# Performance work log

Measured on AMD Instinct MI355X. Metric: run time of the kernel, lower is better.

The kernel has to match this reference:

```python
import jax, jax.numpy as jnp
import numpy as np

N_NODES = 20000
EPS_BN = 1e-5
NEG_SLOPE = 0.2


def gat_conv(x, W, att_src, att_dst, bias, src, dst, heads, out_ch, concat):
    n = x.shape[0]
    h = (x @ W).reshape(n, heads, out_ch)                       # [N,H,C]
    a_src = jnp.sum(h * att_src, axis=-1)                       # [N,H]
    a_dst = jnp.sum(h * att_dst, axis=-1)                       # [N,H]
    e = jax.nn.leaky_relu(a_src[src] + a_dst[dst], NEG_SLOPE)   # [E,H]
    # segment softmax over incoming edges of each destination node
    m = jax.ops.segment_max(e, dst, num_segments=n)             # [N,H]
    e = jnp.exp(e - m[dst])
    denom = jax.ops.segment_sum(e, dst, num_segments=n)         # [N,H]
    alpha = e / (denom[dst] + 1e-16)                            # [E,H]
    msg = alpha[:, :, None] * h[src]                            # [E,H,C]
    out = jax.ops.segment_sum(msg, dst, num_segments=n)         # [N,H,C]
    if concat:
        out = out.reshape(n, heads * out_ch)
    else:
        out = out.mean(axis=1)
    return out + bias


def batch_norm(x, gamma, beta):
    mu = x.mean(axis=0)
    var = x.var(axis=0)  # biased, matches torch normalization
    return (x - mu) * jax.lax.rsqrt(var + EPS_BN) * gamma + beta


def setup_inputs() -> dict:
    key = jax.random.key(0)
    ks = jax.random.split(key, 16)
    n, d_in, hid, heads = N_NODES, 768, 128, 8
    n_edges = 160000
    x = jax.random.normal(ks[0], (n, d_in), dtype=jnp.float32)
    edge_index = jax.random.randint(ks[1], (2, n_edges), 0, n, dtype=jnp.int64)
    s = lambda fi, fo: (2.0 / (fi + fo)) ** 0.5
    return {
        "x": x,
        "edge_index": edge_index,
        "W1": jax.random.normal(ks[2], (d_in, heads * hid), jnp.float32) * s(d_in, heads * hid),
        "att_src1": jax.random.normal(ks[3], (heads, hid), jnp.float32) * 0.1,
        "att_dst1": jax.random.normal(ks[4], (heads, hid), jnp.float32) * 0.1,
        "bias1": jnp.zeros((heads * hid,), jnp.float32),
        "bn1_g": jnp.ones((heads * hid,), jnp.float32),
        "bn1_b": jnp.zeros((heads * hid,), jnp.float32),
        "W2": jax.random.normal(ks[5], (heads * hid, hid), jnp.float32) * s(heads * hid, hid),
        "att_src2": jax.random.normal(ks[6], (1, hid), jnp.float32) * 0.1,
        "att_dst2": jax.random.normal(ks[7], (1, hid), jnp.float32) * 0.1,
        "bias2": jnp.zeros((hid,), jnp.float32),
        "bn2_g": jnp.ones((hid,), jnp.float32),
        "bn2_b": jnp.zeros((hid,), jnp.float32),
        "Wc1": jax.random.normal(ks[8], (hid, 64), jnp.float32) * s(hid, 64),
        "bc1": jnp.zeros((64,), jnp.float32),
        "Wc2": jax.random.normal(ks[9], (64, 2), jnp.float32) * s(64, 2),
        "bc2": jnp.zeros((2,), jnp.float32),
    }


def reference(x, edge_index, W1, att_src1, att_dst1, bias1, bn1_g, bn1_b,
              W2, att_src2, att_dst2, bias2, bn2_g, bn2_b,
              Wc1, bc1, Wc2, bc2):
    n = x.shape[0]
    # PyG GATConv default: add self-loops
    loops = jnp.arange(n, dtype=edge_index.dtype)
    src = jnp.concatenate([edge_index[0], loops])
    dst = jnp.concatenate([edge_index[1], loops])

    h = gat_conv(x, W1, att_src1, att_dst1, bias1, src, dst, heads=8, out_ch=128, concat=True)
    h = jax.nn.elu(batch_norm(h, bn1_g, bn1_b))
    # dropout disabled (deterministic reference)
    h = gat_conv(h, W2, att_src2, att_dst2, bias2, src, dst, heads=1, out_ch=128, concat=False)
    h = jax.nn.elu(batch_norm(h, bn2_g, bn2_b))
    h = jax.nn.elu(h @ Wc1 + bc1)
    return h @ Wc2 + bc2  # [N, 2] logits
```

## Files before the change

kernel.cpp:

```cpp
#include <hip/hip_runtime.h>
#include <stdint.h>

typedef unsigned short u16;
typedef __bf16 bf16x8 __attribute__((ext_vector_type(8)));
typedef float f32x4 __attribute__((ext_vector_type(4)));

__device__ __forceinline__ float b2f(u16 u) {
    unsigned x = ((unsigned)u) << 16;
    return __builtin_bit_cast(float, x);
}
__device__ __forceinline__ u16 f2b(float f) {
    unsigned x = __builtin_bit_cast(unsigned, f);
    x = x + 0x7fffu + ((x >> 16) & 1u);
    return (u16)(x >> 16);
}
__device__ __forceinline__ float leaky(float v) { return v > 0.f ? v : 0.2f * v; }
__device__ __forceinline__ float elu(float v) { return v > 0.f ? v : expm1f(v); }

__device__ __forceinline__ void gload16(const u16* g, u16* l) {
    __builtin_amdgcn_global_load_lds((const __attribute__((address_space(1))) void*)(const void*)g,
                                     (__attribute__((address_space(3))) void*)(void*)l, 16, 0, 0);
}

__global__ void k_cast4(const float* __restrict__ in, u16* __restrict__ out, size_t n4) {
    size_t i = blockIdx.x * (size_t)blockDim.x + threadIdx.x;
    size_t stride = (size_t)gridDim.x * blockDim.x;
    for (; i < n4; i += stride) {
        float4 v = ((const float4*)in)[i];
        ushort4 o;
        o.x = f2b(v.x); o.y = f2b(v.y); o.z = f2b(v.z); o.w = f2b(v.w);
        ((ushort4*)out)[i] = o;
    }
}

__global__ void k_tcast(const float* __restrict__ in, u16* __restrict__ out, int R, int C) {
    __shared__ float tile[32][33];
    int tx = threadIdx.x & 31, ty = threadIdx.x >> 5;
    int c0 = blockIdx.x * 32, r0 = blockIdx.y * 32;
    #pragma unroll
    for (int i = 0; i < 32; i += 8) {
        int r = r0 + ty + i, c = c0 + tx;
        tile[ty + i][tx] = (r < R && c < C) ? in[(size_t)r * C + c] : 0.f;
    }
    __syncthreads();
    #pragma unroll
    for (int i = 0; i < 32; i += 8) {
        int c = c0 + ty + i, r = r0 + tx;
        if (c < C && r < R) out[(size_t)c * R + r] = f2b(tile[tx][ty + i]);
    }
}

#define GBM 128
#define GBN 128
#define GBK 64
#define LDT 72
#define SPLITK 4

__global__ __launch_bounds__(256) void k_gemm(const u16* __restrict__ A, const u16* __restrict__ Bt,
                                              u16* __restrict__ C, int M, int NN, int K, int nCB) {
    __shared__ __align__(16) u16 As[GBM][GBK];
    __shared__ __align__(16) u16 Bs[GBN][GBK];
    int nwg = gridDim.x, orig = blockIdx.x;
    int q = nwg >> 3, r8 = nwg & 7, xcd = orig & 7, sub = orig >> 3;
    int wgid = (xcd < r8 ? xcd * (q + 1) : r8 * (q + 1) + (xcd - r8) * q) + sub;
    int rb = wgid / nCB, cb = wgid % nCB;
    int brow = rb * GBM, bcol = cb * GBN;

    int t = threadIdx.x, lane = t & 63, wid = t >> 6;
    int wm = (wid >> 1) * 64, wn = (wid & 1) * 64;
    int fr = lane & 15, fq = lane >> 4;
    f32x4 acc[4][4] = {};
    int srow = lane >> 3;
    int scol = (((lane & 7) ^ srow)) * 8;
    int dcol = (lane & 7) * 8;
    int nK = K / GBK;
    for (int kt = 0; kt < nK; ++kt) {
        int k0 = kt * GBK;
        #pragma unroll
        for (int cc = 0; cc < 8; ++cc) {
            int c = wid * 8 + cc;
            int r = (c & 15) * 8 + srow;
            if (c < 16) gload16(A + (size_t)(brow + r) * K + k0 + scol, &As[r][dcol]);
            else        gload16(Bt + (size_t)(bcol + r) * K + k0 + scol, &Bs[r][dcol]);
        }
        __syncthreads();
        #pragma unroll
        for (int kk = 0; kk < 2; ++kk) {
            int ko = kk * 32 + fq * 8;
            int kos = ko ^ ((fr & 7) << 3);
            bf16x8 af[4], bg[4];
            #pragma unroll
            for (int i = 0; i < 4; ++i) {
                af[i] = *reinterpret_cast<const bf16x8*>(&As[wm + i * 16 + fr][kos]);
                bg[i] = *reinterpret_cast<const bf16x8*>(&Bs[wn + i * 16 + fr][kos]);
            }
            #pragma unroll
            for (int mi = 0; mi < 4; ++mi)
                #pragma unroll
                for (int ni = 0; ni < 4; ++ni)
                    acc[mi][ni] = __builtin_amdgcn_mfma_f32_16x16x32_bf16(af[mi], bg[ni], acc[mi][ni], 0, 0, 0);
        }
        __syncthreads();
    }
    #pragma unroll
    for (int mi = 0; mi < 4; ++mi) {
        #pragma unroll
        for (int j = 0; j < 4; ++j) {
            int row = brow + wm + mi * 16 + fq * 4 + j;
            if (row < M) {
                #pragma unroll
                for (int ni = 0; ni < 4; ++ni) {
                    int col = bcol + wn + ni * 16 + fr;
                    C[(size_t)row * NN + col] = f2b(acc[mi][ni][j]);
                }
            }
        }
    }
}

__global__ __launch_bounds__(256) void k_gemm2(const u16* __restrict__ A, const u16* __restrict__ Bt,
                                               float* __restrict__ Cp, int M, int K,
                                               const float* __restrict__ scA, const float* __restrict__ shA) {
    __shared__ __align__(16) u16 As[GBM][LDT];
    __shared__ __align__(16) u16 Bs[GBN][LDT];
    int brow = blockIdx.x * GBM;
    int ks = blockIdx.y;
    int kBase = ks * (K / SPLITK);
    int t = threadIdx.x;
    int lane = t & 63, wid = t >> 6;
    int wm = (wid >> 1) * 64, wn = (wid & 1) * 64;
    int fr = lane & 15, fq = lane >> 4;
    f32x4 acc[4][4] = {};
    int tr = t >> 3, tc = (t & 7) * 8;
    const int nK = 1024 / SPLITK / GBK;
    for (int kt = 0; kt < nK; ++kt) {
        int k0 = kBase + kt * GBK;
        #pragma unroll
        for (int rr = 0; rr < 4; ++rr) {
            int r = tr + rr * 32;
            int grow = brow + r;
            uint4 bv = *reinterpret_cast<const uint4*>(Bt + (size_t)r * K + k0 + tc);
            *reinterpret_cast<uint4*>(&Bs[r][tc]) = bv;
            uint4 av = make_uint4(0, 0, 0, 0);
            if (grow < M) {
                uint4 u = *reinterpret_cast<const uint4*>(A + (size_t)grow * K + k0 + tc);
                float4 s0 = *(const float4*)(scA + k0 + tc);
                float4 s1 = *(const float4*)(scA + k0 + tc + 4);
                float4 h0 = *(const float4*)(shA + k0 + tc);
                float4 h1 = *(const float4*)(shA + k0 + tc + 4);
                u16 w0 = f2b(elu(b2f((u16)(u.x & 0xffff)) * s0.x + h0.x));
                u16 w1 = f2b(elu(b2f((u16)(u.x >> 16))    * s0.y + h0.y));
                u16 w2 = f2b(elu(b2f((u16)(u.y & 0xffff)) * s0.z + h0.z));
                u16 w3 = f2b(elu(b2f((u16)(u.y >> 16))    * s0.w + h0.w));
                u16 w4 = f2b(elu(b2f((u16)(u.z & 0xffff)) * s1.x + h1.x));
                u16 w5 = f2b(elu(b2f((u16)(u.z >> 16))    * s1.y + h1.y));
                u16 w6 = f2b(elu(b2f((u16)(u.w & 0xffff)) * s1.z + h1.z));
                u16 w7 = f2b(elu(b2f((u16)(u.w >> 16))    * s1.w + h1.w));
                av.x = (unsigned)w0 | ((unsigned)w1 << 16);
                av.y = (unsigned)w2 | ((unsigned)w3 << 16);
                av.z = (unsigned)w4 | ((unsigned)w5 << 16);
                av.w = (unsigned)w6 | ((unsigned)w7 << 16);
            }
            *reinterpret_cast<uint4*>(&As[r][tc]) = av;
        }
        __syncthreads();
        #pragma unroll
        for (int kk = 0; kk < 2; ++kk) {
            int ko = kk * 32 + fq * 8;
            bf16x8 af[4], bg[4];
            #pragma unroll
            for (int i = 0; i < 4; ++i) {
                af[i] = *reinterpret_cast<const bf16x8*>(&As[wm + i * 16 + fr][ko]);
                bg[i] = *reinterpret_cast<const bf16x8*>(&Bs[wn + i * 16 + fr][ko]);
            }
            #pragma unroll
            for (int mi = 0; mi < 4; ++mi)
                #pragma unroll
                for (int ni = 0; ni < 4; ++ni)
                    acc[mi][ni] = __builtin_amdgcn_mfma_f32_16x16x32_bf16(af[mi], bg[ni], acc[mi][ni], 0, 0, 0);
        }
        __syncthreads();
    }
    float* base = Cp + (size_t)ks * M * 128;
    #pragma unroll
    for (int mi = 0; mi < 4; ++mi) {
        #pragma unroll
        for (int j = 0; j < 4; ++j) {
            int row = brow + wm + mi * 16 + fq * 4 + j;
            if (row < M) {
                #pragma unroll
                for (int ni = 0; ni < 4; ++ni) {
                    int col = wn + ni * 16 + fr;
                    base[(size_t)row * 128 + col] = acc[mi][ni][j];
                }
            }
        }
    }
}

__global__ __launch_bounds__(256) void k_red2(const float* __restrict__ Cp,
                                              const float* __restrict__ attS, const float* __restrict__ attD,
                                              u16* __restrict__ h2b, float* __restrict__ asrc,
                                              float* __restrict__ adst, int M) {
    int t = threadIdx.x, lane = t & 63, wid = t >> 6;
    int row = blockIdx.x * 4 + wid;
    if (row >= M) return;
    int c = lane * 2;
    float s0 = 0.f, s1 = 0.f;
    #pragma unroll
    for (int s = 0; s < SPLITK; ++s) {
        float2 v = *(const float2*)(Cp + ((size_t)s * M + row) * 128 + c);
        s0 += v.x; s1 += v.y;
    }
    ushort2 o; o.x = f2b(s0); o.y = f2b(s1);
    *(ushort2*)(h2b + (size_t)row * 128 + c) = o;
    float ps = s0 * attS[c] + s1 * attS[c + 1];
    float pd = s0 * attD[c] + s1 * attD[c + 1];
    #pragma unroll
    for (int m = 1; m < 64; m <<= 1) { ps += __shfl_xor(ps, m); pd += __shfl_xor(pd, m); }
    if (lane == 0) { asrc[row] = ps; adst[row] = pd; }
}

__global__ void k_att8(const u16* __restrict__ h, const float* __restrict__ attS,
                       const float* __restrict__ attD, float* __restrict__ asrc,
                       float* __restrict__ adst, int N) {
    int t = threadIdx.x;
    int half = t >> 7, i = t & 127;
    int row = blockIdx.x * 2 + half;
    if (row >= N) return;
    int head = i >> 4, g = i & 15;
    const u16* hp = h + (size_t)row * 1024 + head * 128 + g * 8;
    const float* sp = attS + head * 128 + g * 8;
    const float* dp = attD + head * 128 + g * 8;
    ushort4 u0 = *(const ushort4*)hp;
    ushort4 u1 = *(const ushort4*)(hp + 4);
    float hv[8] = {b2f(u0.x), b2f(u0.y), b2f(u0.z), b2f(u0.w),
                   b2f(u1.x), b2f(u1.y), b2f(u1.z), b2f(u1.w)};
    float ps = 0.f, pd = 0.f;
    #pragma unroll
    for (int j = 0; j < 8; ++j) { ps += hv[j] * sp[j]; pd += hv[j] * dp[j]; }
    #pragma unroll
    for (int m = 1; m < 16; m <<= 1) { ps += __shfl_xor(ps, m); pd += __shfl_xor(pd, m); }
    if (g == 0) { asrc[row * 8 + head] = ps; adst[row * 8 + head] = pd; }
}

__global__ void k_detect(const int* __restrict__ ei, int* flag, int E0) {
    if (threadIdx.x == 0) *flag = 0;
    __syncthreads();
    int lim = E0 < 4096 ? E0 : 4096;
    int any = 0;
    for (int i = threadIdx.x; i < lim; i += 256) any |= (ei[2 * i + 1] != 0);
    if (any) atomicOr(flag, 1);
}

__global__ void k_deg(const int* __restrict__ ei, const int* __restrict__ flag,
                      int* __restrict__ deg, int E0, int E) {
    bool i64 = (*flag == 0);
    for (int e = blockIdx.x * blockDim.x + threadIdx.x; e < E; e += gridDim.x * blockDim.x) {
        int d;
        if (e < E0) d = i64 ? ei[2 * (E0 + e)] : ei[E0 + e];
        else d = e - E0;
        atomicAdd(&deg[d], 1);
    }
}

__global__ __launch_bounds__(1024) void k_scan(const int* __restrict__ deg, int* __restrict__ off,
                                               int* __restrict__ cursor, int n) {
    __shared__ int part[1024];
    int t = threadIdx.x;
    int chunk = (n + 1023) >> 10;
    int beg = t * chunk, end = beg + chunk;
    if (end > n) end = n;
    int s = 0;
    for (int i = beg; i < end; ++i) s += deg[i];
    part[t] = s;
    __syncthreads();
    for (int d = 1; d < 1024; d <<= 1) {
        int v = (t >= d) ? part[t - d] : 0;
        __syncthreads();
        part[t] += v;
        __syncthreads();
    }
    int run = (t == 0) ? 0 : part[t - 1];
    for (int i = beg; i < end; ++i) { off[i] = run; cursor[i] = run; run += deg[i]; }
    if (t == 1023) off[n] = part[1023];
}

__global__ void k_scatter(const int* __restrict__ ei, const int* __restrict__ flag,
                          int* __restrict__ cursor, int* __restrict__ csr, int E0, int E) {
    bool i64 = (*flag == 0);
    for (int e = blockIdx.x * blockDim.x + threadIdx.x; e < E; e += gridDim.x * blockDim.x) {
        int s, d;
        if (e < E0) {
            if (i64) { s = ei[2 * e]; d = ei[2 * (E0 + e)]; }
            else     { s = ei[e];     d = ei[E0 + e]; }
        } else { s = d = e - E0; }
        int pos = atomicAdd(&cursor[d], 1);
        csr[pos] = s;
    }
}

template <int HEADS>
__global__ __launch_bounds__(256) void k_alpha(const int* __restrict__ off, const int* __restrict__ csr,
                                               const float* __restrict__ asrc, const float* __restrict__ adst,
                                               float* __restrict__ pbuf, float* __restrict__ invb, int N) {
    const int EPC = 64 / HEADS;
    int t = threadIdx.x, lane = t & 63, wid = t >> 6;
    int node = blockIdx.x * 4 + wid;
    if (node >= N) return;
    int h = lane & (HEADS - 1);
    int e = lane / HEADS;
    float ad = adst[(size_t)node * HEADS + h];
    int lo = off[node], hi = off[node + 1];
    float m = -1e30f;
    for (int i = lo + e; i < hi; i += EPC) {
        int s = csr[i];
        float v = leaky(asrc[(size_t)s * HEADS + h] + ad);
        m = fmaxf(m, v);
    }
    #pragma unroll
    for (int mask = HEADS; mask < 64; mask <<= 1) m = fmaxf(m, __shfl_xor(m, mask));
    float ssum = 0.f;
    for (int i = lo + e; i < hi; i += EPC) {
        int s = csr[i];
        float v = leaky(asrc[(size_t)s * HEADS + h] + ad);
        float p = __expf(v - m);
        pbuf[(size_t)i * HEADS + h] = p;
        ssum += p;
    }
    #pragma unroll
    for (int mask = HEADS; mask < 64; mask <<= 1) ssum += __shfl_xor(ssum, mask);
    if (lane < HEADS) invb[(size_t)node * HEADS + h] = 1.f / (ssum + 1e-16f);
}

__global__ __launch_bounds__(256) void k_agg1(const int* __restrict__ off, const int* __restrict__ csr,
                                              const float* __restrict__ asrc, const float* __restrict__ adst,
                                              const u16* __restrict__ h1, u16* __restrict__ outg, int N) {
    __shared__ float pch[64][8];
    __shared__ float invs[8];
    int node = blockIdx.x;
    if (node >= N) return;
    int t = threadIdx.x, lane = t & 63, wid = t >> 6;
    int hh = t >> 5;
    int c0 = t * 4;
    int lo = off[node], hi = off[node + 1];
    float ad_l = 0.f, mmax = -1e30f, ssum = 0.f;
    int h = lane & 7, es = lane >> 3;
    if (wid == 0) {
        ad_l = adst[(size_t)node * 8 + h];
        for (int i = lo + es; i < hi; i += 8)
            mmax = fmaxf(mmax, leaky(asrc[(size_t)csr[i] * 8 + h] + ad_l));
        #pragma unroll
        for (int mask = 8; mask < 64; mask <<= 1) mmax = fmaxf(mmax, __shfl_xor(mmax, mask));
    }
    float a0 = 0.f, a1 = 0.f, a2 = 0.f, a3 = 0.f;
    for (int base = lo; base < hi; base += 64) {
        int cend = base + 64 < hi ? base + 64 : hi;
        if (wid == 0) {
            for (int i = base + es; i < cend; i += 8) {
                float p = __expf(leaky(asrc[(size_t)csr[i] * 8 + h] + ad_l) - mmax);
                pch[i - base][h] = p;
                ssum += p;
            }
        }
        __syncthreads();
        for (int i = base; i < cend; ++i) {
            float p = pch[i - base][hh];
            ushort4 u = *(const ushort4*)(h1 + (size_t)csr[i] * 1024 + c0);
            a0 += p * b2f(u.x); a1 += p * b2f(u.y);
            a2 += p * b2f(u.z); a3 += p * b2f(u.w);
        }
        __syncthreads();
    }
    if (wid == 0) {
        #pragma unroll
        for (int mask = 8; mask < 64; mask <<= 1) ssum += __shfl_xor(ssum, mask);
        if (lane < 8) invs[lane] = 1.f / (ssum + 1e-16f);
    }
    __syncthreads();
    float inv = invs[hh];
    ushort4 o;
    o.x = f2b(a0 * inv); o.y = f2b(a1 * inv); o.z = f2b(a2 * inv); o.w = f2b(a3 * inv);
    *(ushort4*)(outg + (size_t)node * 1024 + c0) = o;
}

__global__ __launch_bounds__(256) void k_agg2(const int* __restrict__ off, const int* __restrict__ csr,
                                              const float* __restrict__ pbuf, const float* __restrict__ invb,
                                              const u16* __restrict__ h2, u16* __restrict__ outg, int N) {
    int t = threadIdx.x;
    int half = t >> 7, c = t & 127;
    int node = blockIdx.x * 2 + half;
    if (node >= N) return;
    int lo = off[node], hi = off[node + 1];
    float acc = 0.f;
    for (int i = lo; i < hi; ++i) {
        int s = csr[i];
        acc += pbuf[i] * b2f(h2[(size_t)s * 128 + c]);
    }
    outg[(size_t)node * 128 + c] = f2b(acc * invb[node]);
}

template <int CH>
__global__ __launch_bounds__(256) void k_bnpart(const u16* __restrict__ g, float* __restrict__ ps,
                                                float* __restrict__ ps2, int Nrows, int rowsPerChunk) {
    const int TPR = CH / 4;
    const int RPI = 256 / TPR;
    int t = threadIdx.x;
    int rl = t / TPR, c4 = (t % TPR) * 4;
    int chunk = blockIdx.x;
    int r0 = chunk * rowsPerChunk;
    int r1 = r0 + rowsPerChunk; if (r1 > Nrows) r1 = Nrows;
    float s[4] = {0.f, 0.f, 0.f, 0.f}, s2[4] = {0.f, 0.f, 0.f, 0.f};
    for (int r = r0 + rl; r < r1; r += RPI) {
        ushort4 u = *(const ushort4*)(g + (size_t)r * CH + c4);
        float v0 = b2f(u.x), v1 = b2f(u.y), v2 = b2f(u.z), v3 = b2f(u.w);
        s[0] += v0; s2[0] += v0 * v0;
        s[1] += v1; s2[1] += v1 * v1;
        s[2] += v2; s2[2] += v2 * v2;
        s[3] += v3; s2[3] += v3 * v3;
    }
    size_t prow = (size_t)(chunk * RPI + rl) * CH + c4;
    *(float4*)(ps + prow)  = make_float4(s[0], s[1], s[2], s[3]);
    *(float4*)(ps2 + prow) = make_float4(s2[0], s2[1], s2[2], s2[3]);
}

__global__ __launch_bounds__(256) void k_bnfinal(const float* __restrict__ ps, const float* __restrict__ ps2,
                                                 const float* __restrict__ gamma, const float* __restrict__ beta,
                                                 float* __restrict__ scale, float* __restrict__ shift,
                                                 int P, int CH, int Nrows) {
    int t = threadIdx.x, lane = t & 63, wid = t >> 6;
    int col = blockIdx.x * 4 + wid;
    if (col >= CH) return;
    float s = 0.f, s2 = 0.f;
    for (int p = lane; p < P; p += 64) {
        s += ps[(size_t)p * CH + col];
        s2 += ps2[(size_t)p * CH + col];
    }
    #pragma unroll
    for (int m = 1; m < 64; m <<= 1) { s += __shfl_xor(s, m); s2 += __shfl_xor(s2, m); }
    if (lane == 0) {
        double mu = (double)s / Nrows;
        double var = (double)s2 / Nrows - mu * mu;
        if (var < 0) var = 0;
        float sc = gamma[col] * rsqrtf((float)var + 1e-5f);
        scale[col] = sc;
        shift[col] = beta[col] - (float)mu * sc;
    }
}

__global__ __launch_bounds__(256) void k_cls(const u16* __restrict__ g2raw,
                                             const float* __restrict__ scale2, const float* __restrict__ shift2,
                                             const float* __restrict__ Wc1, const float* __restrict__ bc1,
                                             const float* __restrict__ Wc2, const float* __restrict__ bc2,
                                             float* __restrict__ out, int N) {
    __shared__ float wl[128 * 64];
    __shared__ float hs[4][128];
    int t = threadIdx.x, lane = t & 63, wid = t >> 6;
    for (int i = t; i < 128 * 64; i += 256) wl[i] = Wc1[i];
    float sc0 = scale2[2 * lane], sc1 = scale2[2 * lane + 1];
    float sh0 = shift2[2 * lane], sh1 = shift2[2 * lane + 1];
    float bb = bc1[lane];
    float c2a = Wc2[lane * 2], c2b = Wc2[lane * 2 + 1];
    float o2a = bc2[0], o2b = bc2[1];
    __syncthreads();
    int row0 = blockIdx.x * 64;
    for (int it = 0; it < 16; ++it) {
        int row = row0 + it * 4 + wid;
        if (row >= N) continue;
        const u16* hp = g2raw + (size_t)row * 128 + 2 * lane;
        float y0 = b2f(hp[0]) * sc0 + sh0; y0 = y0 > 0.f ? y0 : expm1f(y0);
        float y1 = b2f(hp[1]) * sc1 + sh1; y1 = y1 > 0.f ? y1 : expm1f(y1);
        hs[wid][2 * lane] = y0;
        hs[wid][2 * lane + 1] = y1;
        float tj = bb;
        #pragma unroll 8
        for (int c = 0; c < 128; ++c) tj += hs[wid][c] * wl[c * 64 + lane];
        tj = tj > 0.f ? tj : expm1f(tj);
        float v0 = tj * c2a, v1 = tj * c2b;
        #pragma unroll
        for (int m = 1; m < 64; m <<= 1) { v0 += __shfl_xor(v0, m); v1 += __shfl_xor(v1, m); }
        if (lane == 0) {
            out[(size_t)row * 2 + 0] = v0 + o2a;
            out[(size_t)row * 2 + 1] = v1 + o2b;
        }
    }
}

extern "C" void kernel_launch(void* const* d_in, const int* in_sizes, int n_in,
                              void* d_out, int out_size, void* d_ws, size_t ws_size,
                              hipStream_t stream) {
    const float* x     = (const float*)d_in[0];
    const int*   ei    = (const int*)d_in[1];
    const float* W1    = (const float*)d_in[2];
    const float* attS1 = (const float*)d_in[3];
    const float* attD1 = (const float*)d_in[4];
    const float* bn1g  = (const float*)d_in[6];
    const float* bn1b  = (const float*)d_in[7];
    const float* W2    = (const float*)d_in[8];
    const float* attS2 = (const float*)d_in[9];
    const float* attD2 = (const float*)d_in[10];
    const float* bn2g  = (const float*)d_in[12];
    const float* bn2b  = (const float*)d_in[13];
    const float* Wc1   = (const float*)d_in[14];
    const float* bc1   = (const float*)d_in[15];
    const float* Wc2   = (const float*)d_in[16];
    const float* bc2   = (const float*)d_in[17];
    float* out = (float*)d_out;

    const int DIN = 768, F1 = 1024, C2 = 128;
    const int N = in_sizes[0] / DIN;
    const int E0 = in_sizes[1] / 2;
    const int E = E0 + N;
    const int nMB = (N + GBM - 1) / GBM;
    const int Mp = nMB * GBM;

    char* w = (char*)d_ws;
    auto take = [&](size_t bytes) -> void* {
        void* p = (void*)w;
        w += (bytes + 255) & ~(size_t)255;
        return p;
    };
    u16* xb     = (u16*)take((size_t)Mp * DIN * 2);
    u16* bufA   = (u16*)take((size_t)N * F1 * 2);
    u16* h1b    = (u16*)take((size_t)N * F1 * 2);
    u16* w1t    = (u16*)take((size_t)F1 * DIN * 2);
    u16* w2t    = (u16*)take((size_t)C2 * F1 * 2);
    float* asrc1 = (float*)take((size_t)N * 8 * 4);
    float* adst1 = (float*)take((size_t)N * 8 * 4);
    int* deg    = (int*)take((size_t)N * 4);
    int* off    = (int*)take((size_t)(N + 1) * 4);
    int* cursor = (int*)take((size_t)N * 4);
    int* csr    = (int*)take((size_t)E * 4);
    int* flag   = (int*)take(256);
    u16* h2b    = (u16*)take((size_t)N * C2 * 2);
    float* asrc2 = (float*)take((size_t)N * 4);
    float* adst2 = (float*)take((size_t)N * 4);
    u16* g2     = (u16*)take((size_t)N * C2 * 2);
    float* scale1 = (float*)take(F1 * 4);
    float* shift1 = (float*)take(F1 * 4);
    float* scale2 = (float*)take(C2 * 4);
    float* shift2 = (float*)take(C2 * 4);
    float* pbuf  = (float*)take((size_t)E * 4);
    float* invb2 = (float*)take((size_t)N * 4);
    float* psA   = (float*)take((size_t)1024 * 1024 * 4);
    float* psB   = (float*)take((size_t)1024 * 1024 * 4);
    float* part  = (float*)h1b;

    hipMemsetAsync(deg, 0, (size_t)N * 4, stream);
    k_detect<<<1, 256, 0, stream>>>(ei, flag, E0);

    k_cast4<<<2048, 256, 0, stream>>>(x, xb, (size_t)N * DIN / 4);
    k_tcast<<<dim3(F1 / 32, DIN / 32), 256, 0, stream>>>(W1, w1t, DIN, F1);
    k_tcast<<<dim3(C2 / 32, F1 / 32), 256, 0, stream>>>(W2, w2t, F1, C2);

    k_gemm<<<nMB * (F1 / GBN), 256, 0, stream>>>(xb, w1t, h1b, N, F1, DIN, F1 / GBN);
    k_att8<<<(N + 1) / 2, 256, 0, stream>>>(h1b, attS1, attD1, asrc1, adst1, N);

    k_deg<<<512, 256, 0, stream>>>(ei, flag, deg, E0, E);
    k_scan<<<1, 1024, 0, stream>>>(deg, off, cursor, N);
    k_scatter<<<512, 256, 0, stream>>>(ei, flag, cursor, csr, E0, E);

    k_agg1<<<N, 256, 0, stream>>>(off, csr, asrc1, adst1, h1b, bufA, N);
    {
        int nchunk = 256, rpc = (N + nchunk - 1) / nchunk;
        k_bnpart<1024><<<nchunk, 256, 0, stream>>>(bufA, psA, psB, N, rpc);
        k_bnfinal<<<F1 / 4, 256, 0, stream>>>(psA, psB, bn1g, bn1b, scale1, shift1, nchunk, F1, N);
    }

    k_gemm2<<<dim3(nMB, SPLITK), 256, 0, stream>>>(bufA, w2t, part, N, F1, scale1, shift1);
    k_red2<<<(N + 3) / 4, 256, 0, stream>>>(part, attS2, attD2, h2b, asrc2, adst2, N);

    k_alpha<1><<<(N + 3) / 4, 256, 0, stream>>>(off, csr, asrc2, adst2, pbuf, invb2, N);
    k_agg2<<<(N + 1) / 2, 256, 0, stream>>>(off, csr, pbuf, invb2, h2b, g2, N);
    {
        int nchunk = 128, rpc = (N + nchunk - 1) / nchunk;
        k_bnpart<128><<<nchunk, 256, 0, stream>>>(g2, psA, psB, N, rpc);
        k_bnfinal<<<C2 / 4, 256, 0, stream>>>(psA, psB, bn2g, bn2b, scale2, shift2, nchunk * 8, C2, N);
    }

    k_cls<<<(N + 63) / 64, 256, 0, stream>>>(g2, scale2, shift2, Wc1, bc1, Wc2, bc2, out, N);
}
```

Measured before the change: 366.7 us.

## Fuse x cast into GEMM, merge init and transpose kernels, fuse layer-2 softmax into aggregation

The fp32 to bf16 cast of x now happens inside the first GEMM's A-tile load, using register loads and LDS stores in place of a separate cast pass and async global-to-LDS loads. The memset and format-detect kernels become one, and both weight transposes share a single launch. The layer-2 alpha kernel is folded into k_agg2: one block per node computes the max, exponentials and sum on the fly, which removes the pbuf round trip. The trade-off is that the A tile now goes through registers, losing the async load path and the XOR swizzle (a padded row stride is used instead), and k_agg2 adds extra syncs.

```diff
diff --git a/kernel.cpp b/kernel.cpp
--- a/kernel.cpp
+++ b/kernel.cpp
@@ -22,32 +22,36 @@
                                      (__attribute__((address_space(3))) void*)(void*)l, 16, 0, 0);
 }
 
-__global__ void k_cast4(const float* __restrict__ in, u16* __restrict__ out, size_t n4) {
-    size_t i = blockIdx.x * (size_t)blockDim.x + threadIdx.x;
-    size_t stride = (size_t)gridDim.x * blockDim.x;
-    for (; i < n4; i += stride) {
-        float4 v = ((const float4*)in)[i];
-        ushort4 o;
-        o.x = f2b(v.x); o.y = f2b(v.y); o.z = f2b(v.z); o.w = f2b(v.w);
-        ((ushort4*)out)[i] = o;
-    }
-}
-
-__global__ void k_tcast(const float* __restrict__ in, u16* __restrict__ out, int R, int C) {
+__global__ void k_init(const int* __restrict__ ei, int* __restrict__ flag,
+                       int* __restrict__ deg, int E0, int N) {
+    for (int i = blockIdx.x * blockDim.x + threadIdx.x; i < N; i += gridDim.x * blockDim.x)
+        deg[i] = 0;
+    if (blockIdx.x == 0) {
+        if (threadIdx.x == 0) *flag = 0;
+        __syncthreads();
+        int lim = E0 < 4096 ? E0 : 4096;
+        int any = 0;
+        for (int i = threadIdx.x; i < lim; i += 256) any |= (ei[2 * i + 1] != 0);
+        if (any) atomicOr(flag, 1);
+    }
+}
+
+__global__ void k_tcast2(const float* __restrict__ W1, u16* __restrict__ w1t,
+                         const float* __restrict__ W2, u16* __restrict__ w2t) {
     __shared__ float tile[32][33];
+    int bid = blockIdx.x;
+    const float* in; u16* outp; int R, C, cx, ry;
+    if (bid < 768) { in = W1; outp = w1t; R = 768; C = 1024; cx = bid & 31; ry = bid >> 5; }
+    else { int b = bid - 768; in = W2; outp = w2t; R = 1024; C = 128; cx = b & 3; ry = b >> 2; }
     int tx = threadIdx.x & 31, ty = threadIdx.x >> 5;
-    int c0 = blockIdx.x * 32, r0 = blockIdx.y * 32;
-    #pragma unroll
-    for (int i = 0; i < 32; i += 8) {
-        int r = r0 + ty + i, c = c0 + tx;
-        tile[ty + i][tx] = (r < R && c < C) ? in[(size_t)r * C + c] : 0.f;
-    }
+    int c0 = cx * 32, r0 = ry * 32;
+    #pragma unroll
+    for (int i = 0; i < 32; i += 8)
+        tile[ty + i][tx] = in[(size_t)(r0 + ty + i) * C + c0 + tx];
     __syncthreads();
     #pragma unroll
-    for (int i = 0; i < 32; i += 8) {
-        int c = c0 + ty + i, r = r0 + tx;
-        if (c < C && r < R) out[(size_t)c * R + r] = f2b(tile[tx][ty + i]);
-    }
+    for (int i = 0; i < 32; i += 8)
+        outp[(size_t)(c0 + ty + i) * R + r0 + tx] = f2b(tile[tx][ty + i]);
 }
 
 #define GBM 128
@@ -56,9 +60,9 @@
 #define LDT 72
 #define SPLITK 4
 
-__global__ __launch_bounds__(256) void k_gemm(const u16* __restrict__ A, const u16* __restrict__ Bt,
+__global__ __launch_bounds__(256) void k_gemm(const float* __restrict__ Af, const u16* __restrict__ Bt,
                                               u16* __restrict__ C, int M, int NN, int K, int nCB) {
-    __shared__ __align__(16) u16 As[GBM][GBK];
+    __shared__ __align__(16) u16 As[GBM][LDT];
     __shared__ __align__(16) u16 Bs[GBN][GBK];
     int nwg = gridDim.x, orig = blockIdx.x;
     int q = nwg >> 3, r8 = nwg & 7, xcd = orig & 7, sub = orig >> 3;
@@ -70,18 +74,34 @@
     int wm = (wid >> 1) * 64, wn = (wid & 1) * 64;
     int fr = lane & 15, fq = lane >> 4;
     f32x4 acc[4][4] = {};
+    int tr = t >> 3, tc = (t & 7) * 8;
     int srow = lane >> 3;
-    int scol = (((lane & 7) ^ srow)) * 8;
-    int dcol = (lane & 7) * 8;
+    int scolB = ((lane & 7) ^ srow) * 8;
+    int dcolB = (lane & 7) * 8;
     int nK = K / GBK;
     for (int kt = 0; kt < nK; ++kt) {
         int k0 = kt * GBK;
         #pragma unroll
-        for (int cc = 0; cc < 8; ++cc) {
-            int c = wid * 8 + cc;
-            int r = (c & 15) * 8 + srow;
-            if (c < 16) gload16(A + (size_t)(brow + r) * K + k0 + scol, &As[r][dcol]);
-            else        gload16(Bt + (size_t)(bcol + r) * K + k0 + scol, &Bs[r][dcol]);
+        for (int cc = 0; cc < 4; ++cc) {
+            int g = wid * 4 + cc;
+            int r = g * 8 + srow;
+            gload16(Bt + (size_t)(bcol + r) * K + k0 + scolB, &Bs[r][dcolB]);
+        }
+        #pragma unroll
+        for (int rr = 0; rr < 4; ++rr) {
+            int r = tr + rr * 32;
+            int grow = brow + r;
+            uint4 av = make_uint4(0, 0, 0, 0);
+            if (grow < M) {
+                const float* ap = Af + (size_t)grow * K + k0 + tc;
+                float4 a0 = *(const float4*)ap;
+                float4 a1 = *(const float4*)(ap + 4);
+                av.x = (unsigned)f2b(a0.x) | ((unsigned)f2b(a0.y) << 16);
+                av.y = (unsigned)f2b(a0.z) | ((unsigned)f2b(a0.w) << 16);
+                av.z = (unsigned)f2b(a1.x) | ((unsigned)f2b(a1.y) << 16);
+                av.w = (unsigned)f2b(a1.z) | ((unsigned)f2b(a1.w) << 16);
+            }
+            *reinterpret_cast<uint4*>(&As[r][tc]) = av;
         }
         __syncthreads();
         #pragma unroll
@@ -91,7 +111,7 @@
             bf16x8 af[4], bg[4];
             #pragma unroll
             for (int i = 0; i < 4; ++i) {
-                af[i] = *reinterpret_cast<const bf16x8*>(&As[wm + i * 16 + fr][kos]);
+                af[i] = *reinterpret_cast<const bf16x8*>(&As[wm + i * 16 + fr][ko]);
                 bg[i] = *reinterpret_cast<const bf16x8*>(&Bs[wn + i * 16 + fr][kos]);
             }
             #pragma unroll
@@ -244,15 +264,6 @@
     if (g == 0) { asrc[row * 8 + head] = ps; adst[row * 8 + head] = pd; }
 }
 
-__global__ void k_detect(const int* __restrict__ ei, int* flag, int E0) {
-    if (threadIdx.x == 0) *flag = 0;
-    __syncthreads();
-    int lim = E0 < 4096 ? E0 : 4096;
-    int any = 0;
-    for (int i = threadIdx.x; i < lim; i += 256) any |= (ei[2 * i + 1] != 0);
-    if (any) atomicOr(flag, 1);
-}
-
 __global__ void k_deg(const int* __restrict__ ei, const int* __restrict__ flag,
                       int* __restrict__ deg, int E0, int E) {
     bool i64 = (*flag == 0);
@@ -298,39 +309,6 @@
         int pos = atomicAdd(&cursor[d], 1);
         csr[pos] = s;
     }
-}
-
-template <int HEADS>
-__global__ __launch_bounds__(256) void k_alpha(const int* __restrict__ off, const int* __restrict__ csr,
-                                               const float* __restrict__ asrc, const float* __restrict__ adst,
-                                               float* __restrict__ pbuf, float* __restrict__ invb, int N) {
-    const int EPC = 64 / HEADS;
-    int t = threadIdx.x, lane = t & 63, wid = t >> 6;
-    int node = blockIdx.x * 4 + wid;
-    if (node >= N) return;
-    int h = lane & (HEADS - 1);
-    int e = lane / HEADS;
-    float ad = adst[(size_t)node * HEADS + h];
-    int lo = off[node], hi = off[node + 1];
-    float m = -1e30f;
-    for (int i = lo + e; i < hi; i += EPC) {
-        int s = csr[i];
-        float v = leaky(asrc[(size_t)s * HEADS + h] + ad);
-        m = fmaxf(m, v);
-    }
-    #pragma unroll
-    for (int mask = HEADS; mask < 64; mask <<= 1) m = fmaxf(m, __shfl_xor(m, mask));
-    float ssum = 0.f;
-    for (int i = lo + e; i < hi; i += EPC) {
-        int s = csr[i];
-        float v = leaky(asrc[(size_t)s * HEADS + h] + ad);
-        float p = __expf(v - m);
-        pbuf[(size_t)i * HEADS + h] = p;
-        ssum += p;
-    }
-    #pragma unroll
-    for (int mask = HEADS; mask < 64; mask <<= 1) ssum += __shfl_xor(ssum, mask);
-    if (lane < HEADS) invb[(size_t)node * HEADS + h] = 1.f / (ssum + 1e-16f);
 }
 
 __global__ __launch_bounds__(256) void k_agg1(const int* __restrict__ off, const int* __restrict__ csr,
@@ -384,20 +362,43 @@
     *(ushort4*)(outg + (size_t)node * 1024 + c0) = o;
 }
 
-__global__ __launch_bounds__(256) void k_agg2(const int* __restrict__ off, const int* __restrict__ csr,
-                                              const float* __restrict__ pbuf, const float* __restrict__ invb,
+__global__ __launch_bounds__(128) void k_agg2(const int* __restrict__ off, const int* __restrict__ csr,
+                                              const float* __restrict__ asrc, const float* __restrict__ adst,
                                               const u16* __restrict__ h2, u16* __restrict__ outg, int N) {
-    int t = threadIdx.x;
-    int half = t >> 7, c = t & 127;
-    int node = blockIdx.x * 2 + half;
+    __shared__ float pch[64];
+    __shared__ float invsh;
+    int node = blockIdx.x;
     if (node >= N) return;
+    int t = threadIdx.x, lane = t & 63, wid = t >> 6;
     int lo = off[node], hi = off[node + 1];
+    float ad = adst[node];
+    float mmax = -1e30f, ssum = 0.f;
+    if (wid == 0) {
+        for (int i = lo + lane; i < hi; i += 64)
+            mmax = fmaxf(mmax, leaky(asrc[csr[i]] + ad));
+        #pragma unroll
+        for (int mask = 1; mask < 64; mask <<= 1) mmax = fmaxf(mmax, __shfl_xor(mmax, mask));
+    }
     float acc = 0.f;
-    for (int i = lo; i < hi; ++i) {
-        int s = csr[i];
-        acc += pbuf[i] * b2f(h2[(size_t)s * 128 + c]);
-    }
-    outg[(size_t)node * 128 + c] = f2b(acc * invb[node]);
+    for (int base = lo; base < hi; base += 64) {
+        int cend = base + 64 < hi ? base + 64 : hi;
+        if (wid == 0 && base + lane < cend) {
+            float p = __expf(leaky(asrc[csr[base + lane]] + ad) - mmax);
+            pch[lane] = p;
+            ssum += p;
+        }
+        __syncthreads();
+        for (int i = base; i < cend; ++i)
+            acc += pch[i - base] * b2f(h2[(size_t)csr[i] * 128 + t]);
+        __syncthreads();
+    }
+    if (wid == 0) {
+        #pragma unroll
+        for (int mask = 1; mask < 64; mask <<= 1) ssum += __shfl_xor(ssum, mask);
+        if (lane == 0) invsh = 1.f / (ssum + 1e-16f);
+    }
+    __syncthreads();
+    outg[(size_t)node * 128 + t] = f2b(acc * invsh);
 }
 
 template <int CH>
@@ -512,7 +513,6 @@
     const int E0 = in_sizes[1] / 2;
     const int E = E0 + N;
     const int nMB = (N + GBM - 1) / GBM;
-    const int Mp = nMB * GBM;
 
     char* w = (char*)d_ws;
     auto take = [&](size_t bytes) -> void* {
@@ -520,7 +520,6 @@
         w += (bytes + 255) & ~(size_t)255;
         return p;
     };
-    u16* xb     = (u16*)take((size_t)Mp * DIN * 2);
     u16* bufA   = (u16*)take((size_t)N * F1 * 2);
     u16* h1b    = (u16*)take((size_t)N * F1 * 2);
     u16* w1t    = (u16*)take((size_t)F1 * DIN * 2);
@@ -540,20 +539,14 @@
     float* shift1 = (float*)take(F1 * 4);
     float* scale2 = (float*)take(C2 * 4);
     float* shift2 = (float*)take(C2 * 4);
-    float* pbuf  = (float*)take((size_t)E * 4);
-    float* invb2 = (float*)take((size_t)N * 4);
     float* psA   = (float*)take((size_t)1024 * 1024 * 4);
     float* psB   = (float*)take((size_t)1024 * 1024 * 4);
     float* part  = (float*)h1b;
 
-    hipMemsetAsync(deg, 0, (size_t)N * 4, stream);
-    k_detect<<<1, 256, 0, stream>>>(ei, flag, E0);
-
-    k_cast4<<<2048, 256, 0, stream>>>(x, xb, (size_t)N * DIN / 4);
-    k_tcast<<<dim3(F1 / 32, DIN / 32), 256, 0, stream>>>(W1, w1t, DIN, F1);
-    k_tcast<<<dim3(C2 / 32, F1 / 32), 256, 0, stream>>>(W2, w2t, F1, C2);
-
-    k_gemm<<<nMB * (F1 / GBN), 256, 0, stream>>>(xb, w1t, h1b, N, F1, DIN, F1 / GBN);
+    k_init<<<64, 256, 0, stream>>>(ei, flag, deg, E0, N);
+    k_tcast2<<<768 + 128, 256, 0, stream>>>(W1, w1t, W2, w2t);
+
+    k_gemm<<<nMB * (F1 / GBN), 256, 0, stream>>>(x, w1t, h1b, N, F1, DIN, F1 / GBN);
     k_att8<<<(N + 1) / 2, 256, 0, stream>>>(h1b, attS1, attD1, asrc1, adst1, N);
 
     k_deg<<<512, 256, 0, stream>>>(ei, flag, deg, E0, E);
@@ -570,8 +563,7 @@
     k_gemm2<<<dim3(nMB, SPLITK), 256, 0, stream>>>(bufA, w2t, part, N, F1, scale1, shift1);
     k_red2<<<(N + 3) / 4, 256, 0, stream>>>(part, attS2, attD2, h2b, asrc2, adst2, N);
 
-    k_alpha<1><<<(N + 3) / 4, 256, 0, stream>>>(off, csr, asrc2, adst2, pbuf, invb2, N);
-    k_agg2<<<(N + 1) / 2, 256, 0, stream>>>(off, csr, pbuf, invb2, h2b, g2, N);
+    k_agg2<<<N, 128, 0, stream>>>(off, csr, asrc2, adst2, h2b, g2, N);
     {
         int nchunk = 128, rpc = (N + nchunk - 1) / nchunk;
         k_bnpart<128><<<nchunk, 256, 0, stream>>>(g2, psA, psB, N, rpc);
```

Result: faster. 357.8 us (-2.4%).
